# Performance work log

Hardware: AMD Instinct MI355X
Metric: run time of the kernel (lower is better)

Reference implementation:

```python
import jax, jax.numpy as jnp
import numpy as np

BIG = 1e10  # sentinel for masked-out (padded) points, like pytorch3d's masking


def setup_inputs() -> dict:
    key = jax.random.key(0)
    k1, k2, k3, k4 = jax.random.split(key, 4)
    B, N, M = 16, 4096, 4096
    source_cloud = jax.random.normal(k1, (B, N, 2), dtype=jnp.float32)
    target_cloud = jax.random.normal(k2, (B, M, 2), dtype=jnp.float32)
    source_mask = jax.random.randint(k3, (B,), 0, N)  # lengths1
    target_mask = jax.random.randint(k4, (B,), 0, M)  # lengths2
    return {
        "source_cloud": source_cloud,
        "target_cloud": target_cloud,
        "source_mask": source_mask,
        "target_mask": target_mask,
    }


def reference(source_cloud, target_cloud, source_mask, target_mask):
    # source_cloud: [B, N, 2], target_cloud: [B, M, 2]
    # source_mask/target_mask: int lengths [B] (knn_points lengths1/lengths2)
    B, N, _ = source_cloud.shape
    M = target_cloud.shape[1]

    s2 = jnp.sum(source_cloud * source_cloud, axis=-1)  # [B, N]
    t2 = jnp.sum(target_cloud * target_cloud, axis=-1)  # [B, M]
    # squared pairwise distances [B, N, M]
    d2 = (s2[:, :, None] + t2[:, None, :]
          - 2.0 * jnp.einsum('bnd,bmd->bnm', source_cloud, target_cloud))

    src_valid = jnp.arange(N)[None, :] < source_mask[:, None]  # [B, N]
    tgt_valid = jnp.arange(M)[None, :] < target_mask[:, None]  # [B, M]

    # forward: for each source point, 1-NN over valid target points
    d2_fwd = jnp.where(tgt_valid[:, None, :], d2, BIG)
    min_fwd = jnp.maximum(jnp.min(d2_fwd, axis=-1), 0.0)  # [B, N]
    # backward: for each target point, 1-NN over valid source points
    d2_bwd = jnp.where(src_valid[:, :, None], d2, BIG)
    min_bwd = jnp.maximum(jnp.min(d2_bwd, axis=-2), 0.0)  # [B, M]

    # padded query points get dist 0 (pytorch3d knn_points semantics), then sqrt
    chamfer_forward = jnp.where(src_valid, jnp.sqrt(min_fwd), 0.0)
    chamfer_backward = jnp.where(tgt_valid, jnp.sqrt(min_bwd), 0.0)
    return (chamfer_forward, chamfer_backward)
```

## Files before the change

kernel.cpp:

```cpp
#include <hip/hip_runtime.h>


#define NQ 16

__global__ __launch_bounds__(256, 2) void chamfer_main(
    const float* __restrict__ src, const float* __restrict__ tgt,
    const int* __restrict__ slen, const int* __restrict__ tlen,
    unsigned int* __restrict__ out_bits)
{
    __shared__ float4 sh[256];

    const int bx  = blockIdx.x;
    const int dir = bx >> 8;
    const int b   = (bx >> 4) & 15;
    const int pc  = bx & 15;
    const int tid = threadIdx.x;

    const float* Q = dir ? tgt : src;
    const float* P = dir ? src : tgt;
    const int Lp = dir ? slen[b] : tlen[b];

    {
        const float2 p = ((const float2*)P)[b * 4096 + pc * 256 + tid];
        sh[tid] = make_float4(p.x, p.y, fmaf(p.x, p.x, p.y * p.y), 0.f);
    }
    __syncthreads();

    int count = Lp - pc * 256;
    count = count < 0 ? 0 : (count > 256 ? 256 : count);
    if (count == 0) return;

    float m2x[NQ], m2y[NQ], s2[NQ], best[NQ];
    #pragma unroll
    for (int k = 0; k < NQ; ++k) {
        const float2 q = ((const float2*)Q)[b * 4096 + tid + k * 256];
        m2x[k] = -2.f * q.x;
        m2y[k] = -2.f * q.y;
        s2[k]  = fmaf(q.x, q.x, q.y * q.y);
        best[k] = 3.0e38f;
    }

    #pragma unroll 4
    for (int j = 0; j < count; ++j) {
        const float4 t = sh[j];
        #pragma unroll
        for (int k = 0; k < NQ; ++k) {
            float v = fmaf(m2x[k], t.x, t.z);
            v = fmaf(m2y[k], t.y, v);
            best[k] = fminf(best[k], v);
        }
    }

    unsigned int* row = out_bits + dir * 65536 + b * 4096;
    #pragma unroll
    for (int k = 0; k < NQ; ++k) {
        const float d2 = fmaxf(best[k] + s2[k], 0.f);
        atomicMin(&row[tid + k * 256], __float_as_uint(d2));
    }
}

__global__ __launch_bounds__(256) void chamfer_epilogue(
    unsigned int* __restrict__ out_bits,
    const int* __restrict__ slen, const int* __restrict__ tlen)
{
    const int idx = blockIdx.x * 256 + threadIdx.x;
    const int dir = idx >> 16;
    const int b   = (idx >> 12) & 15;
    const int i   = idx & 4095;
    const int L   = dir ? tlen[b] : slen[b];
    float r = 0.f;
    if (i < L) {
        const unsigned int bits = out_bits[idx];
        r = (bits == 0xFFFFFFFFu) ? 100000.0f
                                  : sqrtf(__uint_as_float(bits));
    }
    ((float*)out_bits)[idx] = r;
}

extern "C" void kernel_launch(void* const* d_in, const int* in_sizes, int n_in,
                              void* d_out, int out_size, void* d_ws, size_t ws_size,
                              hipStream_t stream) {
    const float* src = (const float*)d_in[0];
    const float* tgt = (const float*)d_in[1];
    const int* slen  = (const int*)d_in[2];
    const int* tlen  = (const int*)d_in[3];
    unsigned int* out_bits = (unsigned int*)d_out;

    hipMemsetAsync(out_bits, 0xFF, (size_t)131072 * 4, stream);
    chamfer_main<<<512, 256, 0, stream>>>(src, tgt, slen, tlen, out_bits);
    chamfer_epilogue<<<512, 256, 0, stream>>>(out_bits, slen, tlen);
}
```

Baseline: 90.83 us.

## Use fp16 packed dot products for distances and fuse epilogue via last-block counter

Coordinates are rounded to half precision and packed so that each query–point distance is one fdot2 with an fp32 accumulator, instead of two fp32 FMAs. Points are stored two per shared-memory vector, and padded points get a huge norm so the inner loop can run a fixed trip count. The separate epilogue kernel is removed. A per-row atomic counter lets the last of the 16 blocks in a row apply the sqrt and masking and write the output. This cuts ALU work and one launch, but the fp16 rounding of coordinates adds distance error that may exceed the comparison tolerance.

```diff
diff --git a/kernel.cpp b/kernel.cpp
--- a/kernel.cpp
+++ b/kernel.cpp
@@ -2,13 +2,26 @@
 
 
 #define NQ 16
+typedef _Float16 h2 __attribute__((ext_vector_type(2)));
+
+#if defined(__has_builtin)
+#  if __has_builtin(__builtin_amdgcn_fdot2)
+#    define FDOT2(a, b, c) __builtin_amdgcn_fdot2((a), (b), (c), false)
+#  endif
+#endif
+#ifndef FDOT2
+#  define FDOT2(a, b, c) fmaf((float)(a)[0], (float)(b)[0], fmaf((float)(a)[1], (float)(b)[1], (c)))
+#endif
 
 __global__ __launch_bounds__(256, 2) void chamfer_main(
     const float* __restrict__ src, const float* __restrict__ tgt,
     const int* __restrict__ slen, const int* __restrict__ tlen,
-    unsigned int* __restrict__ out_bits)
+    unsigned int* __restrict__ ws_bits,
+    unsigned int* __restrict__ counters,
+    float* __restrict__ out)
 {
-    __shared__ float4 sh[256];
+    __shared__ float4 sh[128];
+    __shared__ int last_flag;
 
     const int bx  = blockIdx.x;
     const int dir = bx >> 8;
@@ -18,63 +31,81 @@
 
     const float* Q = dir ? tgt : src;
     const float* P = dir ? src : tgt;
+    const int Lq = dir ? tlen[b] : slen[b];
     const int Lp = dir ? slen[b] : tlen[b];
 
-    {
-        const float2 p = ((const float2*)P)[b * 4096 + pc * 256 + tid];
-        sh[tid] = make_float4(p.x, p.y, fmaf(p.x, p.x, p.y * p.y), 0.f);
+    int count = Lp - pc * 256;
+    count = count < 0 ? 0 : (count > 256 ? 256 : count);
+
+    const int row = dir * 16 + b;
+    unsigned int* bits_row = ws_bits + row * 4096;
+
+    if (count > 0) {
+        {
+            const float2 p = ((const float2*)P)[b * 4096 + pc * 256 + tid];
+            h2 th; float t2;
+            if (tid < count) {
+                th = h2{(_Float16)p.x, (_Float16)p.y};
+                const float txf = (float)th[0], tyf = (float)th[1];
+                t2 = fmaf(txf, txf, tyf * tyf);
+            } else {
+                th = h2{(_Float16)0.f, (_Float16)0.f};
+                t2 = 1e30f;
+            }
+            ((float2*)sh)[tid] = make_float2(__builtin_bit_cast(float, th), t2);
+        }
+        __syncthreads();
+
+        h2 qh[NQ]; float s2[NQ], best[NQ];
+        #pragma unroll
+        for (int k = 0; k < NQ; ++k) {
+            const float2 q = ((const float2*)Q)[b * 4096 + tid + k * 256];
+            const _Float16 qx = (_Float16)q.x, qy = (_Float16)q.y;
+            const float qxf = (float)qx, qyf = (float)qy;
+            s2[k]   = fmaf(qxf, qxf, qyf * qyf);
+            qh[k]   = h2{(_Float16)(-2.0f * qxf), (_Float16)(-2.0f * qyf)};
+            best[k] = 3.0e38f;
+        }
+
+        #pragma unroll 2
+        for (int j = 0; j < 128; ++j) {
+            const float4 td = sh[j];
+            const h2 th0 = __builtin_bit_cast(h2, td.x);
+            const h2 th1 = __builtin_bit_cast(h2, td.z);
+            #pragma unroll
+            for (int k = 0; k < NQ; ++k) {
+                const float v0 = FDOT2(qh[k], th0, td.y);
+                const float v1 = FDOT2(qh[k], th1, td.w);
+                best[k] = fminf(best[k], fminf(v0, v1));
+            }
+        }
+
+        #pragma unroll
+        for (int k = 0; k < NQ; ++k) {
+            const float d2 = fmaxf(best[k] + s2[k], 0.f);
+            atomicMin(&bits_row[tid + k * 256], __float_as_uint(d2));
+        }
+    }
+
+    __threadfence();
+    if (tid == 0) {
+        const unsigned int old = atomicAdd(&counters[row], 1u);
+        last_flag = (old == 14u);
     }
     __syncthreads();
 
-    int count = Lp - pc * 256;
-    count = count < 0 ? 0 : (count > 256 ? 256 : count);
-    if (count == 0) return;
-
-    float m2x[NQ], m2y[NQ], s2[NQ], best[NQ];
-    #pragma unroll
-    for (int k = 0; k < NQ; ++k) {
-        const float2 q = ((const float2*)Q)[b * 4096 + tid + k * 256];
-        m2x[k] = -2.f * q.x;
-        m2y[k] = -2.f * q.y;
-        s2[k]  = fmaf(q.x, q.x, q.y * q.y);
-        best[k] = 3.0e38f;
-    }
-
-    #pragma unroll 4
-    for (int j = 0; j < count; ++j) {
-        const float4 t = sh[j];
+    if (last_flag) {
         #pragma unroll
         for (int k = 0; k < NQ; ++k) {
-            float v = fmaf(m2x[k], t.x, t.z);
-            v = fmaf(m2y[k], t.y, v);
-            best[k] = fminf(best[k], v);
+            const int i = tid + k * 256;
+            const unsigned int ubits = atomicMin(&bits_row[i], 0xFFFFFFFFu);
+            float r = 0.f;
+            if (i < Lq)
+                r = (ubits == 0xFFFFFFFFu) ? 100000.0f
+                                           : sqrtf(__uint_as_float(ubits));
+            out[row * 4096 + i] = r;
         }
     }
-
-    unsigned int* row = out_bits + dir * 65536 + b * 4096;
-    #pragma unroll
-    for (int k = 0; k < NQ; ++k) {
-        const float d2 = fmaxf(best[k] + s2[k], 0.f);
-        atomicMin(&row[tid + k * 256], __float_as_uint(d2));
-    }
-}
-
-__global__ __launch_bounds__(256) void chamfer_epilogue(
-    unsigned int* __restrict__ out_bits,
-    const int* __restrict__ slen, const int* __restrict__ tlen)
-{
-    const int idx = blockIdx.x * 256 + threadIdx.x;
-    const int dir = idx >> 16;
-    const int b   = (idx >> 12) & 15;
-    const int i   = idx & 4095;
-    const int L   = dir ? tlen[b] : slen[b];
-    float r = 0.f;
-    if (i < L) {
-        const unsigned int bits = out_bits[idx];
-        r = (bits == 0xFFFFFFFFu) ? 100000.0f
-                                  : sqrtf(__uint_as_float(bits));
-    }
-    ((float*)out_bits)[idx] = r;
 }
 
 extern "C" void kernel_launch(void* const* d_in, const int* in_sizes, int n_in,
@@ -84,9 +115,11 @@
     const float* tgt = (const float*)d_in[1];
     const int* slen  = (const int*)d_in[2];
     const int* tlen  = (const int*)d_in[3];
-    unsigned int* out_bits = (unsigned int*)d_out;
 
-    hipMemsetAsync(out_bits, 0xFF, (size_t)131072 * 4, stream);
-    chamfer_main<<<512, 256, 0, stream>>>(src, tgt, slen, tlen, out_bits);
-    chamfer_epilogue<<<512, 256, 0, stream>>>(out_bits, slen, tlen);
+    unsigned int* ws_bits  = (unsigned int*)d_ws;
+    unsigned int* counters = ws_bits + 131072;
+
+    hipMemsetAsync(d_ws, 0xFF, (size_t)(131072 + 32) * 4, stream);
+    chamfer_main<<<512, 256, 0, stream>>>(src, tgt, slen, tlen,
+                                          ws_bits, counters, (float*)d_out);
 }
```

Result: slower. 124.2 us (+36.8%).
